# Kernel optimization log

Hardware: AMD Instinct MI355X
Metric: run time of the kernel (lower is better)

## Reference

```python
import jax, jax.numpy as jnp
import numpy as np

H = 16
D_MODEL = 2048
D_K = D_MODEL // H


def setup_inputs() -> dict:
    key = jax.random.key(0)
    ks = jax.random.split(key, 5)
    B, S = 4, 2048
    x = jax.random.normal(ks[0], (B, S, D_MODEL), dtype=jnp.float32)
    scale = 1.0 / np.sqrt(D_MODEL)
    Wq = jax.random.normal(ks[1], (D_MODEL, D_MODEL), dtype=jnp.float32) * scale
    Wk = jax.random.normal(ks[2], (D_MODEL, D_MODEL), dtype=jnp.float32) * scale
    Wv = jax.random.normal(ks[3], (D_MODEL, D_MODEL), dtype=jnp.float32) * scale
    Wo = jax.random.normal(ks[4], (D_MODEL, D_MODEL), dtype=jnp.float32) * scale
    return {"x": x, "Wq": Wq, "Wk": Wk, "Wv": Wv, "Wo": Wo, "use_mask": 1}


def reference(x, Wq, Wk, Wv, Wo, use_mask):
    B, S, _ = x.shape
    # nn.Linear with no bias: y = x @ W.T; then split heads -> [B, H, S, d_k]
    def proj(W):
        return (x @ W.T).reshape(B, S, H, D_K).transpose(0, 2, 1, 3)

    q, k, v = proj(Wq), proj(Wk), proj(Wv)
    scores = jnp.einsum("bhqd,bhkd->bhqk", q, k) / jnp.sqrt(jnp.float32(D_K))
    if use_mask:
        causal = jnp.tril(jnp.ones((S, S), dtype=bool))  # [S, S]
        scores = jnp.where(causal, scores, -jnp.inf)
    probs = jax.nn.softmax(scores, axis=-1)
    out = jnp.einsum("bhqk,bhkd->bhqd", probs, v)
    out = out.transpose(0, 2, 1, 3).reshape(B, S, H * D_K)
    return out @ Wo.T
```

## Files before the change

kernel.cpp:

```cpp
#include <hip/hip_runtime.h>
#include <hip/hip_bf16.h>

typedef __bf16 bf16_t;
typedef __bf16 bf16x8 __attribute__((ext_vector_type(8)));
typedef float f32x4 __attribute__((ext_vector_type(4)));

#define B_  4
#define S_  2048
#define H_  16
#define DK_ 128
#define DM_ 2048
#define BS_ (B_ * S_)

static __device__ __forceinline__ f32x4 mfma16(bf16x8 a, bf16x8 b, f32x4 c) {
  return __builtin_amdgcn_mfma_f32_16x16x32_bf16(a, b, c, 0, 0, 0);
}

static __device__ __forceinline__ void async_copy16(const bf16_t* g, bf16_t* l) {
  __builtin_amdgcn_global_load_lds(
      (const __attribute__((address_space(1))) void*)g,
      (__attribute__((address_space(3))) void*)l, 16, 0, 0);
}

#define BARRIER() asm volatile("s_barrier" ::: "memory")

template <int CTRL>
static __device__ __forceinline__ float dpp_rorf(float x) {
  return __builtin_bit_cast(float,
      __builtin_amdgcn_update_dpp(0, __builtin_bit_cast(int, x), CTRL, 0xF, 0xF, true));
}
static __device__ __forceinline__ float rowmax16(float r) {
  r = fmaxf(r, dpp_rorf<0x121>(r));
  r = fmaxf(r, dpp_rorf<0x122>(r));
  r = fmaxf(r, dpp_rorf<0x124>(r));
  r = fmaxf(r, dpp_rorf<0x128>(r));
  return r;
}
static __device__ __forceinline__ float rowsum16(float r) {
  r += dpp_rorf<0x121>(r);
  r += dpp_rorf<0x122>(r);
  r += dpp_rorf<0x124>(r);
  r += dpp_rorf<0x128>(r);
  return r;
}

struct ChainOn  { static constexpr bool v = true;  };
struct ChainOff { static constexpr bool v = false; };

__global__ __launch_bounds__(256) void cvt_bf16(const float* __restrict__ in,
                                                bf16_t* __restrict__ out, int n8) {
  int i = blockIdx.x * 256 + threadIdx.x;
  if (i < n8) {
    const float4* p = (const float4*)in + (size_t)i * 2;
    float4 f0 = p[0], f1 = p[1];
    bf16x8 r;
    r[0] = (bf16_t)f0.x; r[1] = (bf16_t)f0.y; r[2] = (bf16_t)f0.z; r[3] = (bf16_t)f0.w;
    r[4] = (bf16_t)f1.x; r[5] = (bf16_t)f1.y; r[6] = (bf16_t)f1.z; r[7] = (bf16_t)f1.w;
    ((bf16x8*)out)[i] = r;
  }
}

template <typename TC>
static __device__ __forceinline__ void gemm_body(
    const bf16_t* __restrict__ A, const bf16_t* __restrict__ B, TC* __restrict__ C,
    bool vtout, int b256, bf16_t (&Ab)[4][8192], bf16_t (&Bb)[4][8192]) {
  const int tid  = threadIdx.x;
  const int wave = tid >> 6;
  const int lane = tid & 63;
  const int quad = lane >> 4;
  const int l16  = lane & 15;
  const int wm   = (wave >> 2) * 128;
  const int wn   = (wave & 3) * 64;

  const int xcd = b256 & 7;
  const int idx = b256 >> 3;
  const int bm  = (xcd * 4 + (idx >> 3)) * 256;
  const int bn  = (idx & 7) * 256;
  const int K   = DM_;

  const int r0 = wave * 16 + (lane >> 2);
  const int r1 = r0 + 128;
  const int s0 = (r0 + (r0 >> 2)) & 3;
  const int s1 = (r1 + (r1 >> 2)) & 3;
  const size_t aO0 = (size_t)(bm + r0) * K + ((lane & 3) ^ s0) * 8;
  const size_t aO1 = (size_t)(bm + r1) * K + ((lane & 3) ^ s1) * 8;
  const size_t bO0 = (size_t)(bn + r0) * K + ((lane & 3) ^ s0) * 8;
  const size_t bO1 = (size_t)(bn + r1) * K + ((lane & 3) ^ s1) * 8;
  const int dst0 = wave * 512;
  const int dst1 = 4096 + wave * 512;

  auto stage = [&](int slot, int kt) __attribute__((always_inline)) {
    const size_t c = (size_t)kt * 32;
    async_copy16(A + aO0 + c, &Ab[slot][dst0]);
    async_copy16(A + aO1 + c, &Ab[slot][dst1]);
    async_copy16(B + bO0 + c, &Bb[slot][dst0]);
    async_copy16(B + bO1 + c, &Bb[slot][dst1]);
  };

  const int sw = (l16 + (l16 >> 2)) & 3;
  const int qs = (quad ^ sw) * 8;

  f32x4 acc[8][4];
#pragma unroll
  for (int i = 0; i < 8; ++i)
#pragma unroll
    for (int j = 0; j < 4; ++j) acc[i][j] = (f32x4){0.f, 0.f, 0.f, 0.f};

  const int NT = K >> 5;

  stage(0, 0); stage(1, 1); stage(2, 2);
  asm volatile("s_waitcnt vmcnt(8)" ::: "memory");
  BARRIER();

  for (int t = 0; t < NT; ++t) {
    const bf16_t* Abuf = Ab[t & 3];
    const bf16_t* Bbuf = Bb[t & 3];
    const int kt = (t + 3 < NT) ? t + 3 : NT - 1;
    stage((t + 3) & 3, kt);

    bf16x8 af[8], bfr[4];
#pragma unroll
    for (int j = 0; j < 8; ++j)
      af[j] = *(const bf16x8*)(&Abuf[(wm + j * 16 + l16) * 32 + qs]);
#pragma unroll
    for (int n = 0; n < 4; ++n)
      bfr[n] = *(const bf16x8*)(&Bbuf[(wn + n * 16 + l16) * 32 + qs]);

    __builtin_amdgcn_s_setprio(1);
#pragma unroll
    for (int j = 0; j < 8; ++j)
#pragma unroll
      for (int n = 0; n < 4; ++n)
        acc[j][n] = mfma16(af[j], bfr[n], acc[j][n]);
    __builtin_amdgcn_s_setprio(0);

    asm volatile("s_waitcnt vmcnt(8)" ::: "memory");
    BARRIER();
  }

  asm volatile("s_waitcnt vmcnt(0)" ::: "memory");

#pragma unroll
  for (int mt = 0; mt < 8; ++mt)
#pragma unroll
    for (int nt = 0; nt < 4; ++nt)
#pragma unroll
      for (int v = 0; v < 4; ++v) {
        int row = bm + wm + mt * 16 + quad * 4 + v;
        int col = bn + wn + nt * 16 + l16;
        if (vtout) {
          size_t o = (size_t)(((row >> 11) * 16 + (col >> 7)) * 128 + (col & 127)) * S_ +
                     (row & 2047);
          C[o] = (TC)acc[mt][nt][v];
        } else {
          C[(size_t)row * DM_ + col] = (TC)acc[mt][nt][v];
        }
      }
}

__global__ __launch_bounds__(512, 2) void qkv_gemm(
    const bf16_t* __restrict__ xb, const bf16_t* __restrict__ wq,
    const bf16_t* __restrict__ wk, const bf16_t* __restrict__ wv,
    bf16_t* __restrict__ Qb, bf16_t* __restrict__ Kb, bf16_t* __restrict__ Vt) {
  __shared__ bf16_t Ab[4][8192];
  __shared__ bf16_t Bb[4][8192];
  const int seg  = (int)blockIdx.x >> 8;
  const int b256 = (int)blockIdx.x & 255;
  const bf16_t* W = (seg == 0) ? wq : (seg == 1) ? wk : wv;
  bf16_t* C       = (seg == 0) ? Qb : (seg == 1) ? Kb : Vt;
  gemm_body<bf16_t>(xb, W, C, seg == 2, b256, Ab, Bb);
}

__global__ __launch_bounds__(512, 2) void out_gemm(
    const bf16_t* __restrict__ Ob, const bf16_t* __restrict__ Wob,
    float* __restrict__ out) {
  __shared__ bf16_t Ab[4][8192];
  __shared__ bf16_t Bb[4][8192];
  gemm_body<float>(Ob, Wob, out, false, (int)blockIdx.x, Ab, Bb);
}

__global__ __launch_bounds__(256, 2) void attn_kernel(const bf16_t* __restrict__ Q,
                                                      const bf16_t* __restrict__ K,
                                                      const bf16_t* __restrict__ VT,
                                                      bf16_t* __restrict__ O,
                                                      const int* __restrict__ use_mask) {
  __shared__ bf16_t Ks[2 * 64 * 128];
  __shared__ bf16_t Vs[2 * 128 * 64];
  __shared__ bf16_t Ps[2 * 4 * 16 * 64];

  const int tid  = threadIdx.x;
  const int wave = tid >> 6;
  const int lane = tid & 63;
  const int quad = lane >> 4;
  const int l16  = lane & 15;

  const int lid  = (int)(blockIdx.y * gridDim.x + blockIdx.x);
  const int xcd  = lid & 7;
  const int t8   = lid >> 3;
  const int bh   = xcd + ((t8 >> 4) << 3);
  const int pair = t8 & 15;
  const int qa   = 31 - pair;
  const int qc   = pair;
  const int b = bh >> 4, h = bh & 15;
  const int maskflag = *use_mask;

  const size_t qbaseA = ((size_t)b * S_ + (size_t)qa * 64) * DM_ + h * DK_;
  const size_t qbaseC = ((size_t)b * S_ + (size_t)qc * 64) * DM_ + h * DK_;

  int skO[4], svO[4];
#pragma unroll
  for (int p = 0; p < 4; ++p) {
    int rK = p * 16 + wave * 4 + quad;
    skO[p] = rK * DM_ + ((l16 ^ (rK & 7)) * 8);
    int dV = p * 32 + wave * 8 + (lane >> 3);
    svO[p] = dV * S_ + (((lane & 7) ^ (dV & 7)) * 8);
  }

  const bf16_t* Kbase = K + (size_t)b * S_ * DM_ + h * DK_;
  const bf16_t* Vbase = VT + (size_t)bh * DK_ * S_;

  auto stage_kv = [&](int j, int buf) __attribute__((always_inline)) {
    const bf16_t* kb = Kbase + (size_t)j * 64 * DM_;
    const bf16_t* vb = Vbase + (size_t)j * 64;
    bf16_t* kl = Ks + buf * 8192 + wave * 512;
    bf16_t* vl = Vs + buf * 8192 + wave * 512;
#pragma unroll
    for (int p = 0; p < 4; ++p) {
      async_copy16(kb + skO[p], kl + p * 2048);
      async_copy16(vb + svO[p], vl + p * 2048);
    }
  };

  bf16x8 qfA[4], qfC[4];
#pragma unroll
  for (int kk = 0; kk < 4; ++kk) {
    size_t ro = (size_t)(wave * 16 + l16) * DM_ + kk * 32 + quad * 8;
    qfA[kk] = *(const bf16x8*)(Q + qbaseA + ro);
    qfC[kk] = *(const bf16x8*)(Q + qbaseC + ro);
  }

  stage_kv(0, 0);

  f32x4 accA[8], accC[8];
#pragma unroll
  for (int i = 0; i < 8; ++i) {
    accA[i] = (f32x4){0.f, 0.f, 0.f, 0.f};
    accC[i] = (f32x4){0.f, 0.f, 0.f, 0.f};
  }
  float mA[4], lA[4], mC[4], lC[4];
#pragma unroll
  for (int v = 0; v < 4; ++v) {
    mA[v] = -INFINITY; lA[v] = 0.f;
    mC[v] = -INFINITY; lC[v] = 0.f;
  }

  bf16_t* PwA = Ps + wave * 1024;
  bf16_t* PwC = Ps + 4096 + wave * 1024;

  const float c1 = 0.08838834764831845f * 1.4426950408889634f;

  const int ntA = maskflag ? qa + 1 : (S_ / 64);
  const int ntC = maskflag ? qc + 1 : (S_ / 64);

  auto softmax_chain = [&](f32x4 (&s)[4], float (&mrow)[4], float (&lrow)[4],
                           f32x4 (&acc)[8], bf16_t* Pw, bool masked)
      __attribute__((always_inline)) {
#pragma unroll
    for (int v = 0; v < 4; ++v) {
      float x[4];
#pragma unroll
      for (int nt = 0; nt < 4; ++nt) {
        float y = s[nt][v] * c1;
        if (masked) {
          int kg = nt * 16 + l16;
          int qg = wave * 16 + quad * 4 + v;
          if (kg > qg) y = -INFINITY;
        }
        x[nt] = y;
      }
      float r = fmaxf(fmaxf(x[0], x[1]), fmaxf(x[2], x[3]));
      r = rowmax16(r);
      float m = mrow[v];
      if (r > m + 8.f) {
        float alpha = __builtin_amdgcn_exp2f(m - r);
        lrow[v] *= alpha;
#pragma unroll
        for (int dt = 0; dt < 8; ++dt) acc[dt][v] *= alpha;
        mrow[v] = r;
        m = r;
      }
      float rs = 0.f;
      int prow = quad * 4 + v;
#pragma unroll
      for (int nt = 0; nt < 4; ++nt) {
        float p = __builtin_amdgcn_exp2f(x[nt] - m);
        rs += p;
        Pw[prow * 64 + ((nt * 16 + l16) ^ ((prow & 7) << 3))] = (bf16_t)p;
      }
      lrow[v] += rowsum16(rs);
    }
  };

  auto body = [&](auto DOC, int cur, bool maskedA, bool maskedC)
      __attribute__((always_inline)) {
    constexpr bool doC = decltype(DOC)::v;
    const bf16_t* KsB = Ks + cur * 8192;
    const bf16_t* VsB = Vs + cur * 8192;

    f32x4 sA[4], sC[4];
#pragma unroll
    for (int nt = 0; nt < 4; ++nt) {
      sA[nt] = (f32x4){0.f, 0.f, 0.f, 0.f};
      sC[nt] = (f32x4){0.f, 0.f, 0.f, 0.f};
    }
    __builtin_amdgcn_s_setprio(1);
#pragma unroll
    for (int kk = 0; kk < 4; ++kk) {
#pragma unroll
      for (int nt = 0; nt < 4; ++nt) {
        bf16x8 kf = *(const bf16x8*)(KsB + (nt * 16 + l16) * 128 +
                                     ((kk * 32 + quad * 8) ^ ((l16 & 7) << 3)));
        sA[nt] = mfma16(qfA[kk], kf, sA[nt]);
        if constexpr (doC) sC[nt] = mfma16(qfC[kk], kf, sC[nt]);
      }
    }
    __builtin_amdgcn_s_setprio(0);

    softmax_chain(sA, mA, lA, accA, PwA, maskedA);
    if constexpr (doC) softmax_chain(sC, mC, lC, accC, PwC, maskedC);

    __builtin_amdgcn_s_setprio(1);
#pragma unroll
    for (int kk = 0; kk < 2; ++kk) {
      bf16x8 pfA = *(const bf16x8*)(PwA + l16 * 64 +
                                    ((kk * 32 + quad * 8) ^ ((l16 & 7) << 3)));
      bf16x8 pfC = {};
      if constexpr (doC)
        pfC = *(const bf16x8*)(PwC + l16 * 64 +
                               ((kk * 32 + quad * 8) ^ ((l16 & 7) << 3)));
#pragma unroll
      for (int dt = 0; dt < 8; ++dt) {
        bf16x8 vf = *(const bf16x8*)(VsB + (dt * 16 + l16) * 64 +
                                     ((kk * 32 + quad * 8) ^ ((l16 & 7) << 3)));
        accA[dt] = mfma16(pfA, vf, accA[dt]);
        if constexpr (doC) accC[dt] = mfma16(pfC, vf, accC[dt]);
      }
    }
    __builtin_amdgcn_s_setprio(0);
  };

  __syncthreads();

  for (int t = 0; t < ntA; ++t) {
    const int cur = t & 1;
    if (t + 1 < ntA) stage_kv(t + 1, cur ^ 1);
    const bool mAf = maskflag && (t == qa);
    if (t < ntC)
      body(ChainOn{},  cur, mAf, maskflag && (t == qc));
    else
      body(ChainOff{}, cur, mAf, false);
    __syncthreads();
  }

  auto epilogue = [&](f32x4 (&acc)[8], float (&lrow)[4], size_t qbase)
      __attribute__((always_inline)) {
    float rl[4];
#pragma unroll
    for (int v = 0; v < 4; ++v) rl[v] = __builtin_amdgcn_rcpf(lrow[v]);
#pragma unroll
    for (int dt = 0; dt < 8; ++dt)
#pragma unroll
      for (int v = 0; v < 4; ++v) {
        int qr = wave * 16 + quad * 4 + v;
        O[qbase + (size_t)qr * DM_ + dt * 16 + l16] = (bf16_t)(acc[dt][v] * rl[v]);
      }
  };
  epilogue(accA, lA, qbaseA);
  epilogue(accC, lC, qbaseC);
}

extern "C" void kernel_launch(void* const* d_in, const int* in_sizes, int n_in,
                              void* d_out, int out_size, void* d_ws, size_t ws_size,
                              hipStream_t stream) {
  const float* x  = (const float*)d_in[0];
  const float* Wq = (const float*)d_in[1];
  const float* Wk = (const float*)d_in[2];
  const float* Wv = (const float*)d_in[3];
  const float* Wo = (const float*)d_in[4];
  const int* use_mask = (const int*)d_in[5];
  float* out = (float*)d_out;

  const size_t TSZ = (size_t)BS_ * DM_;
  const size_t WSZ = (size_t)DM_ * DM_;
  bf16_t* Qb  = (bf16_t*)d_ws;
  bf16_t* Kb  = Qb + TSZ;
  bf16_t* Vt  = Kb + TSZ;
  bf16_t* xb  = Vt + TSZ;
  bf16_t* Ob  = xb;
  bf16_t* Wob = Vt;
  bf16_t* wq = (bf16_t*)d_out;
  bf16_t* wk = wq + WSZ;
  bf16_t* wv = wk + WSZ;

  cvt_bf16<<<(int)(TSZ / 8 / 256), 256, 0, stream>>>(x,  xb, (int)(TSZ / 8));
  cvt_bf16<<<(int)(WSZ / 8 / 256), 256, 0, stream>>>(Wq, wq, (int)(WSZ / 8));
  cvt_bf16<<<(int)(WSZ / 8 / 256), 256, 0, stream>>>(Wk, wk, (int)(WSZ / 8));
  cvt_bf16<<<(int)(WSZ / 8 / 256), 256, 0, stream>>>(Wv, wv, (int)(WSZ / 8));

  qkv_gemm<<<dim3(768), 512, 0, stream>>>(xb, wq, wk, wv, Qb, Kb, Vt);

  dim3 gA(16, 64);
  attn_kernel<<<gA, 256, 0, stream>>>(Qb, Kb, Vt, Ob, use_mask);

  cvt_bf16<<<(int)(WSZ / 8 / 256), 256, 0, stream>>>(Wo, Wob, (int)(WSZ / 8));
  out_gemm<<<dim3(256), 512, 0, stream>>>(Ob, Wob, out);
}
```

Baseline: 654.9 us.

## Restructure GEMM main loop into fine-grained interleaved half-tile load/compute schedule

The projection GEMMs now use a 64-wide K step split into two 32-wide halves, double-buffered. The loop is unrolled over two K tiles, each split into four sub-phases per M half. Each sub-phase issues a small async A or B copy, loads half the A fragments, and runs 16 MFMAs, instead of loading all fragments and running 32 MFMAs per barrier. The aim is to spread global-to-LDS traffic between MFMA bursts and cut register pressure from A fragments. In exchange it adds many more barriers, and the vmcnt(6) accounting is delicate.

```diff
diff --git a/kernel.cpp b/kernel.cpp
--- a/kernel.cpp
+++ b/kernel.cpp
@@ -23,6 +23,7 @@
 }
 
 #define BARRIER() asm volatile("s_barrier" ::: "memory")
+#define WAIT_VM6() asm volatile("s_waitcnt vmcnt(6)" ::: "memory")
 
 template <int CTRL>
 static __device__ __forceinline__ float dpp_rorf(float x) {
@@ -63,7 +64,7 @@
 template <typename TC>
 static __device__ __forceinline__ void gemm_body(
     const bf16_t* __restrict__ A, const bf16_t* __restrict__ B, TC* __restrict__ C,
-    bool vtout, int b256, bf16_t (&Ab)[4][8192], bf16_t (&Bb)[4][8192]) {
+    bool vtout, int b256, bf16_t (&Ab)[2][2][8192], bf16_t (&Bb)[2][2][8192]) {
   const int tid  = threadIdx.x;
   const int wave = tid >> 6;
   const int lane = tid & 63;
@@ -89,12 +90,15 @@
   const int dst0 = wave * 512;
   const int dst1 = 4096 + wave * 512;
 
-  auto stage = [&](int slot, int kt) __attribute__((always_inline)) {
-    const size_t c = (size_t)kt * 32;
-    async_copy16(A + aO0 + c, &Ab[slot][dst0]);
-    async_copy16(A + aO1 + c, &Ab[slot][dst1]);
-    async_copy16(B + bO0 + c, &Bb[slot][dst0]);
-    async_copy16(B + bO1 + c, &Bb[slot][dst1]);
+  auto stA = [&](int buf, int kh, int kt) __attribute__((always_inline)) {
+    const size_t c = (size_t)kt * 64 + kh * 32;
+    async_copy16(A + aO0 + c, &Ab[buf][kh][dst0]);
+    async_copy16(A + aO1 + c, &Ab[buf][kh][dst1]);
+  };
+  auto stB = [&](int buf, int kh, int kt) __attribute__((always_inline)) {
+    const size_t c = (size_t)kt * 64 + kh * 32;
+    async_copy16(B + bO0 + c, &Bb[buf][kh][dst0]);
+    async_copy16(B + bO1 + c, &Bb[buf][kh][dst1]);
   };
 
   const int sw = (l16 + (l16 >> 2)) & 3;
@@ -106,36 +110,73 @@
 #pragma unroll
     for (int j = 0; j < 4; ++j) acc[i][j] = (f32x4){0.f, 0.f, 0.f, 0.f};
 
-  const int NT = K >> 5;
-
-  stage(0, 0); stage(1, 1); stage(2, 2);
-  asm volatile("s_waitcnt vmcnt(8)" ::: "memory");
-  BARRIER();
-
-  for (int t = 0; t < NT; ++t) {
-    const bf16_t* Abuf = Ab[t & 3];
-    const bf16_t* Bbuf = Bb[t & 3];
-    const int kt = (t + 3 < NT) ? t + 3 : NT - 1;
-    stage((t + 3) & 3, kt);
-
-    bf16x8 af[8], bfr[4];
-#pragma unroll
-    for (int j = 0; j < 8; ++j)
-      af[j] = *(const bf16x8*)(&Abuf[(wm + j * 16 + l16) * 32 + qs]);
+  bf16x8 af[4], bfr[4];
+
+  auto lda = [&](int buf, int kh, int mh) __attribute__((always_inline)) {
+#pragma unroll
+    for (int i = 0; i < 4; ++i)
+      af[i] = *(const bf16x8*)(&Ab[buf][kh][(wm + mh * 64 + i * 16 + l16) * 32 + qs]);
+  };
+  auto ldb = [&](int buf, int kh) __attribute__((always_inline)) {
 #pragma unroll
     for (int n = 0; n < 4; ++n)
-      bfr[n] = *(const bf16x8*)(&Bbuf[(wn + n * 16 + l16) * 32 + qs]);
-
+      bfr[n] = *(const bf16x8*)(&Bb[buf][kh][(wn + n * 16 + l16) * 32 + qs]);
+  };
+  auto mma = [&](int mh) __attribute__((always_inline)) {
     __builtin_amdgcn_s_setprio(1);
 #pragma unroll
-    for (int j = 0; j < 8; ++j)
+    for (int i = 0; i < 4; ++i)
 #pragma unroll
       for (int n = 0; n < 4; ++n)
-        acc[j][n] = mfma16(af[j], bfr[n], acc[j][n]);
+        acc[mh * 4 + i][n] = mfma16(af[i], bfr[n], acc[mh * 4 + i][n]);
     __builtin_amdgcn_s_setprio(0);
-
-    asm volatile("s_waitcnt vmcnt(8)" ::: "memory");
-    BARRIER();
+  };
+
+  const int NT    = K >> 6;
+  const int ITERS = NT >> 1;
+
+  stB(0, 0, 0); stA(0, 0, 0); stB(0, 1, 0); stA(0, 1, 0);
+  stB(1, 0, 1); stA(1, 0, 1); stB(1, 1, 1);
+
+  for (int I = 0; I < ITERS; ++I) {
+    const int o   = 2 * I + 1;
+    const int te2 = (2 * I + 2 < NT) ? 2 * I + 2 : NT - 1;
+    const int to2 = (2 * I + 3 < NT) ? 2 * I + 3 : NT - 1;
+
+    WAIT_VM6();
+    BARRIER();
+    lda(0, 0, 0); ldb(0, 0);
+    stA(1, 1, o);
+    mma(0);
+    BARRIER();
+    lda(0, 0, 1);
+    stB(0, 0, te2);
+    mma(1);
+    BARRIER();
+    lda(0, 1, 0); ldb(0, 1);
+    stA(0, 0, te2);
+    mma(0);
+    BARRIER();
+    lda(0, 1, 1);
+    stB(0, 1, te2);
+    mma(1);
+    WAIT_VM6();
+    BARRIER();
+    lda(1, 0, 0); ldb(1, 0);
+    stA(0, 1, te2);
+    mma(0);
+    BARRIER();
+    lda(1, 0, 1);
+    stB(1, 0, to2);
+    mma(1);
+    BARRIER();
+    lda(1, 1, 0); ldb(1, 1);
+    stA(1, 0, to2);
+    mma(0);
+    BARRIER();
+    lda(1, 1, 1);
+    stB(1, 1, to2);
+    mma(1);
   }
 
   asm volatile("s_waitcnt vmcnt(0)" ::: "memory");
@@ -162,8 +203,8 @@
     const bf16_t* __restrict__ xb, const bf16_t* __restrict__ wq,
     const bf16_t* __restrict__ wk, const bf16_t* __restrict__ wv,
     bf16_t* __restrict__ Qb, bf16_t* __restrict__ Kb, bf16_t* __restrict__ Vt) {
-  __shared__ bf16_t Ab[4][8192];
-  __shared__ bf16_t Bb[4][8192];
+  __shared__ bf16_t Ab[2][2][8192];
+  __shared__ bf16_t Bb[2][2][8192];
   const int seg  = (int)blockIdx.x >> 8;
   const int b256 = (int)blockIdx.x & 255;
   const bf16_t* W = (seg == 0) ? wq : (seg == 1) ? wk : wv;
@@ -174,8 +215,8 @@
 __global__ __launch_bounds__(512, 2) void out_gemm(
     const bf16_t* __restrict__ Ob, const bf16_t* __restrict__ Wob,
     float* __restrict__ out) {
-  __shared__ bf16_t Ab[4][8192];
-  __shared__ bf16_t Bb[4][8192];
+  __shared__ bf16_t Ab[2][2][8192];
+  __shared__ bf16_t Bb[2][2][8192];
   gemm_body<float>(Ob, Wob, out, false, (int)blockIdx.x, Ab, Bb);
 }
 
```

Result: faster. 601.2 us (-8.2%).

## Software-pipeline GEMM main loop with split A-fragment reads interleaved with MFMAs

Applied to the files above, without the earlier changes.

Restructures the shared GEMM main loop (used by the QKV and output projections) into an unrolled 4-phase schedule. LDS fragment reads for the next step are issued between two halves of the MFMA block, and register banks are double-buffered. Global offsets become 32-bit relative to a block base pointer. The goal is to hide LDS read latency behind matrix math, at the cost of more barriers per K-step, higher register pressure, and a more intricate buffer-reuse ordering that could race.

```diff
diff --git a/kernel.cpp b/kernel.cpp
--- a/kernel.cpp
+++ b/kernel.cpp
@@ -23,6 +23,7 @@
 }
 
 #define BARRIER() asm volatile("s_barrier" ::: "memory")
+#define WAIT_VM4() asm volatile("s_waitcnt vmcnt(4)" ::: "memory")
 
 template <int CTRL>
 static __device__ __forceinline__ float dpp_rorf(float x) {
@@ -63,7 +64,7 @@
 template <typename TC>
 static __device__ __forceinline__ void gemm_body(
     const bf16_t* __restrict__ A, const bf16_t* __restrict__ B, TC* __restrict__ C,
-    bool vtout, int b256, bf16_t (&Ab)[4][8192], bf16_t (&Bb)[4][8192]) {
+    bool vtout, int b256, bf16_t (&Ab)[2][2][8192], bf16_t (&Bb)[2][2][8192]) {
   const int tid  = threadIdx.x;
   const int wave = tid >> 6;
   const int lane = tid & 63;
@@ -78,23 +79,23 @@
   const int bn  = (idx & 7) * 256;
   const int K   = DM_;
 
-  const int r0 = wave * 16 + (lane >> 2);
-  const int r1 = r0 + 128;
-  const int s0 = (r0 + (r0 >> 2)) & 3;
-  const int s1 = (r1 + (r1 >> 2)) & 3;
-  const size_t aO0 = (size_t)(bm + r0) * K + ((lane & 3) ^ s0) * 8;
-  const size_t aO1 = (size_t)(bm + r1) * K + ((lane & 3) ^ s1) * 8;
-  const size_t bO0 = (size_t)(bn + r0) * K + ((lane & 3) ^ s0) * 8;
-  const size_t bO1 = (size_t)(bn + r1) * K + ((lane & 3) ^ s1) * 8;
+  const bf16_t* Ablk = A + (size_t)bm * (size_t)K;
+  const bf16_t* Bblk = B + (size_t)bn * (size_t)K;
+  const int r0  = wave * 16 + (lane >> 2);
+  const int r1  = r0 + 128;
+  const int sz0 = (r0 + (r0 >> 2)) & 3;
+  const int sz1 = (r1 + (r1 >> 2)) & 3;
+  const int o0  = r0 * K + (((lane & 3) ^ sz0) * 8);
+  const int o1  = r1 * K + (((lane & 3) ^ sz1) * 8);
   const int dst0 = wave * 512;
   const int dst1 = 4096 + wave * 512;
 
-  auto stage = [&](int slot, int kt) __attribute__((always_inline)) {
-    const size_t c = (size_t)kt * 32;
-    async_copy16(A + aO0 + c, &Ab[slot][dst0]);
-    async_copy16(A + aO1 + c, &Ab[slot][dst1]);
-    async_copy16(B + bO0 + c, &Bb[slot][dst0]);
-    async_copy16(B + bO1 + c, &Bb[slot][dst1]);
+  auto stg = [&](int buf, int kh, int kt) __attribute__((always_inline)) {
+    const int c = kt * 64 + kh * 32;
+    async_copy16(Ablk + o0 + c, &Ab[buf][kh][dst0]);
+    async_copy16(Ablk + o1 + c, &Ab[buf][kh][dst1]);
+    async_copy16(Bblk + o0 + c, &Bb[buf][kh][dst0]);
+    async_copy16(Bblk + o1 + c, &Bb[buf][kh][dst1]);
   };
 
   const int sw = (l16 + (l16 >> 2)) & 3;
@@ -106,35 +107,87 @@
 #pragma unroll
     for (int j = 0; j < 4; ++j) acc[i][j] = (f32x4){0.f, 0.f, 0.f, 0.f};
 
-  const int NT = K >> 5;
-
-  stage(0, 0); stage(1, 1); stage(2, 2);
+  bf16x8 af0[2][4], bf[2][4], af1[4];
+
+  auto rdA0 = [&](int bank, int buf, int kh) __attribute__((always_inline)) {
+#pragma unroll
+    for (int i = 0; i < 4; ++i)
+      af0[bank][i] = *(const bf16x8*)(&Ab[buf][kh][(wm + i * 16 + l16) * 32 + qs]);
+  };
+  auto rdA1 = [&](int buf, int kh) __attribute__((always_inline)) {
+#pragma unroll
+    for (int i = 0; i < 4; ++i)
+      af1[i] = *(const bf16x8*)(&Ab[buf][kh][(wm + 64 + i * 16 + l16) * 32 + qs]);
+  };
+  auto rdB = [&](int bank, int buf, int kh) __attribute__((always_inline)) {
+#pragma unroll
+    for (int n = 0; n < 4; ++n)
+      bf[bank][n] = *(const bf16x8*)(&Bb[buf][kh][(wn + n * 16 + l16) * 32 + qs]);
+  };
+  auto mma0 = [&](int bank) __attribute__((always_inline)) {
+    __builtin_amdgcn_s_setprio(1);
+#pragma unroll
+    for (int i = 0; i < 4; ++i)
+#pragma unroll
+      for (int n = 0; n < 4; ++n)
+        acc[i][n] = mfma16(af0[bank][i], bf[bank][n], acc[i][n]);
+    __builtin_amdgcn_s_setprio(0);
+  };
+  auto mma1 = [&](int bank) __attribute__((always_inline)) {
+    __builtin_amdgcn_s_setprio(1);
+#pragma unroll
+    for (int i = 0; i < 4; ++i)
+#pragma unroll
+      for (int n = 0; n < 4; ++n)
+        acc[4 + i][n] = mfma16(af1[i], bf[bank][n], acc[4 + i][n]);
+    __builtin_amdgcn_s_setprio(0);
+  };
+
+  const int NT = K >> 6;
+
+  stg(0, 0, 0); stg(0, 1, 0); stg(1, 0, 1);
   asm volatile("s_waitcnt vmcnt(8)" ::: "memory");
   BARRIER();
-
-  for (int t = 0; t < NT; ++t) {
-    const bf16_t* Abuf = Ab[t & 3];
-    const bf16_t* Bbuf = Bb[t & 3];
-    const int kt = (t + 3 < NT) ? t + 3 : NT - 1;
-    stage((t + 3) & 3, kt);
-
-    bf16x8 af[8], bfr[4];
-#pragma unroll
-    for (int j = 0; j < 8; ++j)
-      af[j] = *(const bf16x8*)(&Abuf[(wm + j * 16 + l16) * 32 + qs]);
-#pragma unroll
-    for (int n = 0; n < 4; ++n)
-      bfr[n] = *(const bf16x8*)(&Bbuf[(wn + n * 16 + l16) * 32 + qs]);
-
-    __builtin_amdgcn_s_setprio(1);
-#pragma unroll
-    for (int j = 0; j < 8; ++j)
-#pragma unroll
-      for (int n = 0; n < 4; ++n)
-        acc[j][n] = mfma16(af[j], bfr[n], acc[j][n]);
-    __builtin_amdgcn_s_setprio(0);
-
-    asm volatile("s_waitcnt vmcnt(8)" ::: "memory");
+  rdA0(0, 0, 0); rdB(0, 0, 0);
+  asm volatile("s_waitcnt vmcnt(4)" ::: "memory");
+  BARRIER();
+
+  for (int I = 0; I < (NT >> 1); ++I) {
+    const int o   = 2 * I + 1;
+    const int te2 = (2 * I + 2 < NT) ? 2 * I + 2 : NT - 1;
+    const int to2 = (2 * I + 3 < NT) ? 2 * I + 3 : NT - 1;
+
+    rdA1(0, 0);
+    stg(1, 1, o);
+    BARRIER();
+    mma0(0);
+    rdA0(1, 0, 1); rdB(1, 0, 1);
+    mma1(0);
+    WAIT_VM4();
+    BARRIER();
+    rdA1(0, 1);
+    stg(0, 0, te2);
+    BARRIER();
+    mma0(1);
+    rdA0(0, 1, 0); rdB(0, 1, 0);
+    mma1(1);
+    WAIT_VM4();
+    BARRIER();
+    rdA1(1, 0);
+    stg(0, 1, te2);
+    BARRIER();
+    mma0(0);
+    rdA0(1, 1, 1); rdB(1, 1, 1);
+    mma1(0);
+    WAIT_VM4();
+    BARRIER();
+    rdA1(1, 1);
+    stg(1, 0, to2);
+    BARRIER();
+    mma0(1);
+    rdA0(0, 0, 0); rdB(0, 0, 0);
+    mma1(1);
+    WAIT_VM4();
     BARRIER();
   }
 
@@ -162,8 +215,8 @@
     const bf16_t* __restrict__ xb, const bf16_t* __restrict__ wq,
     const bf16_t* __restrict__ wk, const bf16_t* __restrict__ wv,
     bf16_t* __restrict__ Qb, bf16_t* __restrict__ Kb, bf16_t* __restrict__ Vt) {
-  __shared__ bf16_t Ab[4][8192];
-  __shared__ bf16_t Bb[4][8192];
+  __shared__ bf16_t Ab[2][2][8192];
+  __shared__ bf16_t Bb[2][2][8192];
   const int seg  = (int)blockIdx.x >> 8;
   const int b256 = (int)blockIdx.x & 255;
   const bf16_t* W = (seg == 0) ? wq : (seg == 1) ? wk : wv;
@@ -174,8 +227,8 @@
 __global__ __launch_bounds__(512, 2) void out_gemm(
     const bf16_t* __restrict__ Ob, const bf16_t* __restrict__ Wob,
     float* __restrict__ out) {
-  __shared__ bf16_t Ab[4][8192];
-  __shared__ bf16_t Bb[4][8192];
+  __shared__ bf16_t Ab[2][2][8192];
+  __shared__ bf16_t Bb[2][2][8192];
   gemm_body<float>(Ob, Wob, out, false, (int)blockIdx.x, Ab, Bb);
 }
 
```

After: 591.7 us. 1.11x faster.
